# Kernel tuning notes

Hardware: AMD Instinct MI355X
Metric: run time of the kernel (lower is better)

The kernel has to match this reference:

```python
import jax, jax.numpy as jnp
import numpy as np

N_HEADS = 12
HIDDEN = 768
HEAD_DIM = HIDDEN // N_HEADS
B, S = 4, 2048


def setup_inputs() -> dict:
    key = jax.random.key(0)
    ks = jax.random.split(key, 7)
    bound = 1.0 / np.sqrt(HIDDEN)  # torch nn.Linear default init range
    inputs = jax.random.normal(ks[0], (B, S, HIDDEN), dtype=jnp.float32)
    Wq = jax.random.uniform(ks[1], (HIDDEN, HIDDEN), jnp.float32, -bound, bound)
    bq = jax.random.uniform(ks[2], (HIDDEN,), jnp.float32, -bound, bound)
    Wk = jax.random.uniform(ks[3], (HIDDEN, HIDDEN), jnp.float32, -bound, bound)
    bk = jax.random.uniform(ks[4], (HIDDEN,), jnp.float32, -bound, bound)
    Wv = jax.random.uniform(ks[5], (HIDDEN, HIDDEN), jnp.float32, -bound, bound)
    bv = jax.random.uniform(ks[6], (HIDDEN,), jnp.float32, -bound, bound)
    return {"inputs": inputs, "Wq": Wq, "bq": bq, "Wk": Wk, "bk": bk, "Wv": Wv, "bv": bv}


def reference(inputs, Wq, bq, Wk, bk, Wv, bv):
    b, s, d = inputs.shape
    h, hd = N_HEADS, HEAD_DIM
    # torch Linear: x @ W^T + b; reshape to (b, s, h, hd) -> (b, h, s, hd)
    def proj(W, bias):
        y = inputs @ W.T + bias
        return y.reshape(b, s, h, hd).transpose(0, 2, 1, 3)
    q = proj(Wq, bq)
    k = proj(Wk, bk)
    v = proj(Wv, bv)
    scale = 1.0 / jnp.sqrt(jnp.asarray(hd, inputs.dtype))
    scores = jnp.einsum('bhqd,bhkd->bhqk', q, k) * scale  # [b,h,s,s] materialized as in source
    attn = jax.nn.softmax(scores, axis=-1)
    out = jnp.einsum('bhqk,bhkd->bhqd', attn, v)
    # (b, h, s, hd) -> (b, s, h*hd)
    return out.transpose(0, 2, 1, 3).reshape(b, s, d)
```

## Files before the change

### kernel.cpp

```cpp
#include <hip/hip_runtime.h>
#include <hip/hip_bf16.h>
#include <math.h>

#define NH   12
#define HD   64
#define HID  768
#define NB   4
#define SS   2048
#define MR   (NB*SS)

#define NXE  (MR*HID)
#define NWE  (HID*HID)

typedef unsigned short u16;
typedef u16   u16x8  __attribute__((ext_vector_type(8)));
typedef __bf16 bf16x8 __attribute__((ext_vector_type(8)));
typedef float f32x4  __attribute__((ext_vector_type(4)));

__device__ __forceinline__ float hi2f(unsigned u) {
    union { unsigned i; float f; } c; c.i = u & 0xffff0000u; return c.f;
}
__device__ __forceinline__ float lo2f(unsigned u) {
    union { unsigned i; float f; } c; c.i = u << 16; return c.f;
}
__device__ __forceinline__ u16 f2b(float f) {
    union { float f; unsigned i; } c; c.f = f;
    unsigned x = c.i + 0x7fffu + ((c.i >> 16) & 1u);
    return (u16)(x >> 16);
}
__device__ __forceinline__ unsigned pk2(float lo, float hi) {
    float2 f; f.x = lo; f.y = hi;
    union { __hip_bfloat162 h; unsigned u; } c;
    c.h = __float22bfloat162_rn(f);
    return c.u;
}
__device__ __forceinline__ f32x4 mfma16(u16x8 a, u16x8 b, f32x4 c) {
    return __builtin_amdgcn_mfma_f32_16x16x32_bf16(
        __builtin_bit_cast(bf16x8, a), __builtin_bit_cast(bf16x8, b), c, 0, 0, 0);
}
__device__ __forceinline__ void g2l16(const u16* g, u16* l) {
    __builtin_amdgcn_global_load_lds(
        (const __attribute__((address_space(1))) void*)g,
        (__attribute__((address_space(3))) void*)l, 16, 0, 0);
}
__device__ __forceinline__ int kperm(int k) {
    return ((k >> 5) << 5) | (((k >> 2) & 1) << 4) | (((k >> 3) & 3) << 2) | (k & 3);
}

__global__ __launch_bounds__(256) void to_bf16(
    const float* __restrict__ x,  const float* __restrict__ Wq,
    const float* __restrict__ Wk, const float* __restrict__ Wv,
    u16* __restrict__ dst)
{
    const int NX4 = NXE / 4, NW4 = NWE / 4, NT4 = NX4 + 3 * NW4;
    for (int i = blockIdx.x * 256 + threadIdx.x; i < NT4; i += gridDim.x * 256) {
        const float* src; u16* d;
        if (i < NX4) { src = x + (size_t)i * 4; d = dst + (size_t)i * 4; }
        else {
            int j = i - NX4; int w = j / NW4; int r = j - w * NW4;
            const float* Ws = (w == 0) ? Wq : ((w == 1) ? Wk : Wv);
            src = Ws + (size_t)r * 4; d = dst + NXE + (size_t)w * NWE + (size_t)r * 4;
        }
        float4 f = *(const float4*)src;
        uint2 o; o.x = pk2(f.x, f.y); o.y = pk2(f.z, f.w);
        *(uint2*)d = o;
    }
}

__global__ __launch_bounds__(256, 3) void qkv_proj(
    const u16* __restrict__ xb, const u16* __restrict__ Wb,
    const float* __restrict__ bq, const float* __restrict__ bk,
    const float* __restrict__ bv, u16* __restrict__ qkv)
{
    const int wsel = blockIdx.z;
    const u16* W = Wb + (size_t)wsel * NWE;
    const float* bias = (wsel == 0) ? bq : ((wsel == 1) ? bk : bv);
    u16* out = qkv + (size_t)wsel * MR * HID;

    const int m0 = blockIdx.x * 128, n0 = blockIdx.y * 128;
    __shared__ __align__(16) u16 As[128][32];
    __shared__ __align__(16) u16 Bs[128][32];

    const int tid  = threadIdx.x;
    const int lane = tid & 63, wid = tid >> 6;
    const int quad = lane >> 4, l16 = lane & 15;
    const int wm = wid >> 1, wn = wid & 1;

    const int rA = 2 * wid * 16 + (lane >> 2);
    const int colh = (lane & 3) * 8;
    const u16* gx0 = xb + (size_t)(m0 + rA) * HID + colh;
    const u16* gx1 = gx0 + (size_t)16 * HID;
    const u16* gw0 = W  + (size_t)(n0 + rA) * HID + colh;
    const u16* gw1 = gw0 + (size_t)16 * HID;
    u16* lA0 = &As[0][0] + (2 * wid) * 512 + lane * 8;
    u16* lA1 = lA0 + 512;
    u16* lB0 = &Bs[0][0] + (2 * wid) * 512 + lane * 8;
    u16* lB1 = lB0 + 512;

    f32x4 acc[4][4] = {};

    for (int k0 = 0; k0 < HID; k0 += 32) {
        g2l16(gx0 + k0, lA0); g2l16(gx1 + k0, lA1);
        g2l16(gw0 + k0, lB0); g2l16(gw1 + k0, lB1);
        __syncthreads();
        u16x8 af[4], bf[4];
        #pragma unroll
        for (int i = 0; i < 4; i++) af[i] = *(const u16x8*)&As[wm * 64 + i * 16 + l16][quad * 8];
        #pragma unroll
        for (int j = 0; j < 4; j++) bf[j] = *(const u16x8*)&Bs[wn * 64 + j * 16 + l16][quad * 8];
        #pragma unroll
        for (int i = 0; i < 4; i++)
            #pragma unroll
            for (int j = 0; j < 4; j++)
                acc[i][j] = mfma16(af[i], bf[j], acc[i][j]);
        __syncthreads();
    }

    if (wsel == 2) {
        const int bidx = m0 >> 11;
        const int s0 = (m0 & 2047) + wm * 64;
        #pragma unroll
        for (int j = 0; j < 4; j++) {
            const int col = n0 + wn * 64 + j * 16 + l16;
            const float bb = bias[col];
            const int hh = col >> 6, d = col & 63;
            u16* vrow = out + ((size_t)(bidx * NH + hh) * HD + d) * SS;
            #pragma unroll
            for (int i = 0; i < 4; i++) {
                uint2 pk;
                pk.x = pk2(acc[i][j][0] + bb, acc[i][j][1] + bb);
                pk.y = pk2(acc[i][j][2] + bb, acc[i][j][3] + bb);
                *(uint2*)(vrow + s0 + i * 16 + quad * 4) = pk;
            }
        }
    } else {
        const float scale = (wsel == 0) ? 0.18033688f : 1.0f;
        #pragma unroll
        for (int j = 0; j < 4; j++) {
            const int col = n0 + wn * 64 + j * 16 + l16;
            const float bb = bias[col];
            #pragma unroll
            for (int i = 0; i < 4; i++)
                #pragma unroll
                for (int r = 0; r < 4; r++) {
                    int row = m0 + wm * 64 + i * 16 + quad * 4 + r;
                    if (wsel == 1) row = (row & ~63) | kperm(row & 63);
                    out[(size_t)row * HID + col] = f2b((acc[i][j][r] + bb) * scale);
                }
        }
    }
}

__global__ __launch_bounds__(256, 3) void attn(
    const u16* __restrict__ qkv, float* __restrict__ out)
{
    const int q0 = blockIdx.x * 128;
    const int h  = blockIdx.y;
    const int b  = blockIdx.z;

    const u16* qb  = qkv + (size_t)b * SS * HID + h * HD;
    const u16* kb  = qkv + (size_t)MR * HID + (size_t)b * SS * HID + h * HD;
    const u16* vtb = qkv + (size_t)2 * MR * HID + ((size_t)(b * NH + h) * HD) * SS;
    float*     ob  = out + (size_t)b * SS * HID + h * HD;

    __shared__ __align__(16) u16 Ks[64][72];
    __shared__ __align__(16) u16 Vt[64][72];

    const int tid  = threadIdx.x;
    const int lane = tid & 63, wid = tid >> 6;
    const int quad = lane >> 4, l16 = lane & 15;
    const int srow = tid >> 3, scg = tid & 7;

    u16x8 qf[2][2];
    #pragma unroll
    for (int t = 0; t < 2; t++) {
        const int row = q0 + t * 64 + wid * 16 + l16;
        #pragma unroll
        for (int hh = 0; hh < 2; hh++)
            qf[t][hh] = *(const u16x8*)(qb + (size_t)row * HID + hh * 32 + quad * 8);
    }

    f32x4 o2[2][4] = {};
    float lsum[2] = {0.f, 0.f};

    for (int kt = 0; kt < SS / 64; kt++) {
        #pragma unroll
        for (int r2 = 0; r2 < 2; r2++) {
            const int rr = r2 * 32 + srow;
            *(uint4*)&Ks[rr][scg * 8] =
                *(const uint4*)(kb + (size_t)(kt * 64 + rr) * HID + scg * 8);
            *(uint4*)&Vt[rr][scg * 8] =
                *(const uint4*)(vtb + (size_t)rr * SS + kt * 64 + scg * 8);
        }
        __syncthreads();

        u16x8 kf[4][2];
        #pragma unroll
        for (int n = 0; n < 4; n++)
            #pragma unroll
            for (int hh = 0; hh < 2; hh++)
                kf[n][hh] = *(const u16x8*)&Ks[n * 16 + l16][hh * 32 + quad * 8];

        unsigned pkd[2][4][2];
        #pragma unroll
        for (int t = 0; t < 2; t++)
            #pragma unroll
            for (int n = 0; n < 4; n++) {
                f32x4 s = {};
                s = mfma16(kf[n][0], qf[t][0], s);
                s = mfma16(kf[n][1], qf[t][1], s);
                const float p0 = __builtin_amdgcn_exp2f(s[0] - 6.0f);
                const float p1 = __builtin_amdgcn_exp2f(s[1] - 6.0f);
                const float p2 = __builtin_amdgcn_exp2f(s[2] - 6.0f);
                const float p3 = __builtin_amdgcn_exp2f(s[3] - 6.0f);
                const unsigned w01 = pk2(p0, p1);
                const unsigned w23 = pk2(p2, p3);
                pkd[t][n][0] = w01; pkd[t][n][1] = w23;
                lsum[t] += (lo2f(w01) + hi2f(w01)) + (lo2f(w23) + hi2f(w23));
            }

        u16x8 vf[4][2];
        #pragma unroll
        for (int n2 = 0; n2 < 4; n2++)
            #pragma unroll
            for (int hh = 0; hh < 2; hh++)
                vf[n2][hh] = *(const u16x8*)&Vt[n2 * 16 + l16][hh * 32 + quad * 8];

        #pragma unroll
        for (int t = 0; t < 2; t++) {
            union { u16x8 v; unsigned d[4]; } bf0, bf1;
            bf0.d[0] = pkd[t][0][0]; bf0.d[1] = pkd[t][0][1];
            bf0.d[2] = pkd[t][1][0]; bf0.d[3] = pkd[t][1][1];
            bf1.d[0] = pkd[t][2][0]; bf1.d[1] = pkd[t][2][1];
            bf1.d[2] = pkd[t][3][0]; bf1.d[3] = pkd[t][3][1];
            #pragma unroll
            for (int n2 = 0; n2 < 4; n2++) {
                o2[t][n2] = mfma16(vf[n2][0], bf0.v, o2[t][n2]);
                o2[t][n2] = mfma16(vf[n2][1], bf1.v, o2[t][n2]);
            }
        }
        __syncthreads();
    }

    #pragma unroll
    for (int t = 0; t < 2; t++) {
        float rs = lsum[t];
        rs += __shfl_xor(rs, 16);
        rs += __shfl_xor(rs, 32);
        const float inv = 1.f / rs;
        const int q = q0 + t * 64 + wid * 16 + l16;
        #pragma unroll
        for (int n2 = 0; n2 < 4; n2++) {
            f32x4 w = o2[t][n2];
            w[0] *= inv; w[1] *= inv; w[2] *= inv; w[3] *= inv;
            *(f32x4*)(ob + (size_t)q * HID + n2 * 16 + quad * 4) = w;
        }
    }
}

extern "C" void kernel_launch(void* const* d_in, const int* in_sizes, int n_in,
                              void* d_out, int out_size, void* d_ws, size_t ws_size,
                              hipStream_t stream) {
    const float* x  = (const float*)d_in[0];
    const float* Wq = (const float*)d_in[1];
    const float* bq = (const float*)d_in[2];
    const float* Wk = (const float*)d_in[3];
    const float* bk = (const float*)d_in[4];
    const float* Wv = (const float*)d_in[5];
    const float* bv = (const float*)d_in[6];
    float* out = (float*)d_out;
    u16* qkv = (u16*)d_ws;
    u16* cvt = (u16*)d_out;

    to_bf16<<<1024, 256, 0, stream>>>(x, Wq, Wk, Wv, cvt);

    dim3 gp(MR / 128, HID / 128, 3);
    qkv_proj<<<gp, 256, 0, stream>>>(cvt, cvt + NXE, bq, bk, bv, qkv);

    dim3 ga(SS / 128, NH, NB);
    attn<<<ga, 256, 0, stream>>>(qkv, out);
}
```

Baseline: 206.5 us.

## Double-buffer K/V tiles, compute row sums via MFMA, stage V transpose through LDS

The attention kernel now double-buffers K and V tiles in shared memory and prefetches the next tile into registers, so global loads overlap compute and only one barrier per iteration remains. Softmax row sums are accumulated by an MFMA against a vector of ones, replacing scalar unpack-and-add plus shuffles, and the -6 offset is folded into the accumulator's initial value. The QKV projection now stages the transposed V output through shared memory so global writes are 16-byte coalesced. The cost is more shared memory and register pressure, which may lower occupancy.

Result: slower. 247.5 us (+19.9%).

```diff
diff --git a/kernel.cpp b/kernel.cpp
--- a/kernel.cpp
+++ b/kernel.cpp
@@ -78,8 +78,9 @@
     u16* out = qkv + (size_t)wsel * MR * HID;
 
     const int m0 = blockIdx.x * 128, n0 = blockIdx.y * 128;
-    __shared__ __align__(16) u16 As[128][32];
-    __shared__ __align__(16) u16 Bs[128][32];
+    __shared__ __align__(16) u16 smem[18432];
+    u16 (*As)[32] = (u16(*)[32])smem;
+    u16 (*Bs)[32] = (u16(*)[32])(smem + 4096);
 
     const int tid  = threadIdx.x;
     const int lane = tid & 63, wid = tid >> 6;
@@ -92,9 +93,9 @@
     const u16* gx1 = gx0 + (size_t)16 * HID;
     const u16* gw0 = W  + (size_t)(n0 + rA) * HID + colh;
     const u16* gw1 = gw0 + (size_t)16 * HID;
-    u16* lA0 = &As[0][0] + (2 * wid) * 512 + lane * 8;
+    u16* lA0 = smem + (2 * wid) * 512 + lane * 8;
     u16* lA1 = lA0 + 512;
-    u16* lB0 = &Bs[0][0] + (2 * wid) * 512 + lane * 8;
+    u16* lB0 = smem + 4096 + (2 * wid) * 512 + lane * 8;
     u16* lB1 = lB0 + 512;
 
     f32x4 acc[4][4] = {};
@@ -117,21 +118,29 @@
     }
 
     if (wsel == 2) {
-        const int bidx = m0 >> 11;
-        const int s0 = (m0 & 2047) + wm * 64;
+        u16* lt = smem + wid * 4608;
         #pragma unroll
         for (int j = 0; j < 4; j++) {
             const int col = n0 + wn * 64 + j * 16 + l16;
             const float bb = bias[col];
-            const int hh = col >> 6, d = col & 63;
-            u16* vrow = out + ((size_t)(bidx * NH + hh) * HD + d) * SS;
             #pragma unroll
             for (int i = 0; i < 4; i++) {
                 uint2 pk;
                 pk.x = pk2(acc[i][j][0] + bb, acc[i][j][1] + bb);
                 pk.y = pk2(acc[i][j][2] + bb, acc[i][j][3] + bb);
-                *(uint2*)(vrow + s0 + i * 16 + quad * 4) = pk;
+                *(uint2*)(lt + (j * 16 + l16) * 72 + i * 16 + quad * 4) = pk;
             }
+        }
+        __syncthreads();
+        const int bidx = m0 >> 11;
+        const int s0 = (m0 & 2047) + wm * 64;
+        #pragma unroll
+        for (int it = 0; it < 8; it++) {
+            const int dl = it * 8 + (lane >> 3), sl = (lane & 7) * 8;
+            uint4 w = *(const uint4*)(lt + dl * 72 + sl);
+            const int col = n0 + wn * 64 + dl;
+            const int hh = col >> 6, d = col & 63;
+            *(uint4*)(out + ((size_t)(bidx * NH + hh) * HD + d) * SS + s0 + sl) = w;
         }
     } else {
         const float scale = (wsel == 0) ? 0.18033688f : 1.0f;
@@ -163,13 +172,14 @@
     const u16* vtb = qkv + (size_t)2 * MR * HID + ((size_t)(b * NH + h) * HD) * SS;
     float*     ob  = out + (size_t)b * SS * HID + h * HD;
 
-    __shared__ __align__(16) u16 Ks[64][72];
-    __shared__ __align__(16) u16 Vt[64][72];
+    __shared__ __align__(16) u16 Ks[2][64][72];
+    __shared__ __align__(16) u16 Vt[2][64][72];
 
     const int tid  = threadIdx.x;
     const int lane = tid & 63, wid = tid >> 6;
     const int quad = lane >> 4, l16 = lane & 15;
     const int srow = tid >> 3, scg = tid & 7;
+    const int rr0 = srow, rr1 = 32 + srow;
 
     u16x8 qf[2][2];
     #pragma unroll
@@ -180,51 +190,69 @@
             qf[t][hh] = *(const u16x8*)(qb + (size_t)row * HID + hh * 32 + quad * 8);
     }
 
+    u16x8 ones;
+    #pragma unroll
+    for (int e = 0; e < 8; e++) ones[e] = 0x3F80;
+
     f32x4 o2[2][4] = {};
-    float lsum[2] = {0.f, 0.f};
+    f32x4 lacc[2] = {};
+
+    uint4 kreg[2], vreg[2];
+    kreg[0] = *(const uint4*)(kb + (size_t)rr0 * HID + scg * 8);
+    kreg[1] = *(const uint4*)(kb + (size_t)rr1 * HID + scg * 8);
+    vreg[0] = *(const uint4*)(vtb + (size_t)rr0 * SS + scg * 8);
+    vreg[1] = *(const uint4*)(vtb + (size_t)rr1 * SS + scg * 8);
+    *(uint4*)&Ks[0][rr0][scg * 8] = kreg[0];
+    *(uint4*)&Ks[0][rr1][scg * 8] = kreg[1];
+    *(uint4*)&Vt[0][rr0][scg * 8] = vreg[0];
+    *(uint4*)&Vt[0][rr1][scg * 8] = vreg[1];
+    kreg[0] = *(const uint4*)(kb + (size_t)(64 + rr0) * HID + scg * 8);
+    kreg[1] = *(const uint4*)(kb + (size_t)(64 + rr1) * HID + scg * 8);
+    vreg[0] = *(const uint4*)(vtb + (size_t)rr0 * SS + 64 + scg * 8);
+    vreg[1] = *(const uint4*)(vtb + (size_t)rr1 * SS + 64 + scg * 8);
+    __syncthreads();
 
     for (int kt = 0; kt < SS / 64; kt++) {
-        #pragma unroll
-        for (int r2 = 0; r2 < 2; r2++) {
-            const int rr = r2 * 32 + srow;
-            *(uint4*)&Ks[rr][scg * 8] =
-                *(const uint4*)(kb + (size_t)(kt * 64 + rr) * HID + scg * 8);
-            *(uint4*)&Vt[rr][scg * 8] =
-                *(const uint4*)(vtb + (size_t)rr * SS + kt * 64 + scg * 8);
-        }
-        __syncthreads();
-
-        u16x8 kf[4][2];
+        const int cur = kt & 1;
+
+        u16x8 kf[4][2], vf[4][2];
         #pragma unroll
         for (int n = 0; n < 4; n++)
             #pragma unroll
-            for (int hh = 0; hh < 2; hh++)
-                kf[n][hh] = *(const u16x8*)&Ks[n * 16 + l16][hh * 32 + quad * 8];
+            for (int hh = 0; hh < 2; hh++) {
+                kf[n][hh] = *(const u16x8*)&Ks[cur][n * 16 + l16][hh * 32 + quad * 8];
+                vf[n][hh] = *(const u16x8*)&Vt[cur][n * 16 + l16][hh * 32 + quad * 8];
+            }
+
+        if (kt < 31) {
+            *(uint4*)&Ks[cur ^ 1][rr0][scg * 8] = kreg[0];
+            *(uint4*)&Ks[cur ^ 1][rr1][scg * 8] = kreg[1];
+            *(uint4*)&Vt[cur ^ 1][rr0][scg * 8] = vreg[0];
+            *(uint4*)&Vt[cur ^ 1][rr1][scg * 8] = vreg[1];
+        }
+        if (kt < 30) {
+            const int kn = (kt + 2) * 64;
+            kreg[0] = *(const uint4*)(kb + (size_t)(kn + rr0) * HID + scg * 8);
+            kreg[1] = *(const uint4*)(kb + (size_t)(kn + rr1) * HID + scg * 8);
+            vreg[0] = *(const uint4*)(vtb + (size_t)rr0 * SS + kn + scg * 8);
+            vreg[1] = *(const uint4*)(vtb + (size_t)rr1 * SS + kn + scg * 8);
+        }
 
         unsigned pkd[2][4][2];
         #pragma unroll
         for (int t = 0; t < 2; t++)
             #pragma unroll
             for (int n = 0; n < 4; n++) {
-                f32x4 s = {};
+                f32x4 s = {-6.f, -6.f, -6.f, -6.f};
                 s = mfma16(kf[n][0], qf[t][0], s);
                 s = mfma16(kf[n][1], qf[t][1], s);
-                const float p0 = __builtin_amdgcn_exp2f(s[0] - 6.0f);
-                const float p1 = __builtin_amdgcn_exp2f(s[1] - 6.0f);
-                const float p2 = __builtin_amdgcn_exp2f(s[2] - 6.0f);
-                const float p3 = __builtin_amdgcn_exp2f(s[3] - 6.0f);
-                const unsigned w01 = pk2(p0, p1);
-                const unsigned w23 = pk2(p2, p3);
-                pkd[t][n][0] = w01; pkd[t][n][1] = w23;
-                lsum[t] += (lo2f(w01) + hi2f(w01)) + (lo2f(w23) + hi2f(w23));
+                const float p0 = __builtin_amdgcn_exp2f(s[0]);
+                const float p1 = __builtin_amdgcn_exp2f(s[1]);
+                const float p2 = __builtin_amdgcn_exp2f(s[2]);
+                const float p3 = __builtin_amdgcn_exp2f(s[3]);
+                pkd[t][n][0] = pk2(p0, p1);
+                pkd[t][n][1] = pk2(p2, p3);
             }
-
-        u16x8 vf[4][2];
-        #pragma unroll
-        for (int n2 = 0; n2 < 4; n2++)
-            #pragma unroll
-            for (int hh = 0; hh < 2; hh++)
-                vf[n2][hh] = *(const u16x8*)&Vt[n2 * 16 + l16][hh * 32 + quad * 8];
 
         #pragma unroll
         for (int t = 0; t < 2; t++) {
@@ -233,21 +261,20 @@
             bf0.d[2] = pkd[t][1][0]; bf0.d[3] = pkd[t][1][1];
             bf1.d[0] = pkd[t][2][0]; bf1.d[1] = pkd[t][2][1];
             bf1.d[2] = pkd[t][3][0]; bf1.d[3] = pkd[t][3][1];
+            lacc[t] = mfma16(ones, bf0.v, lacc[t]);
+            lacc[t] = mfma16(ones, bf1.v, lacc[t]);
             #pragma unroll
             for (int n2 = 0; n2 < 4; n2++) {
                 o2[t][n2] = mfma16(vf[n2][0], bf0.v, o2[t][n2]);
                 o2[t][n2] = mfma16(vf[n2][1], bf1.v, o2[t][n2]);
             }
         }
-        __syncthreads();
+        if (kt < 31) __syncthreads();
     }
 
     #pragma unroll
     for (int t = 0; t < 2; t++) {
-        float rs = lsum[t];
-        rs += __shfl_xor(rs, 16);
-        rs += __shfl_xor(rs, 32);
-        const float inv = 1.f / rs;
+        const float inv = 1.f / lacc[t][0];
         const int q = q0 + t * 64 + wid * 16 + l16;
         #pragma unroll
         for (int n2 = 0; n2 < 4; n2++) {
```
